# Kernel tuning notes

Measured on AMD Instinct MI355X. Metric: run time of the kernel, lower is better.

The kernel has to match this reference:

```python
import jax, jax.numpy as jnp
import numpy as np

B = 1024
P = 8
D = 2048
NUM_IDS = 64
MARGIN = 0.3
EPS = 1e-12


def setup_inputs() -> dict:
    key = jax.random.key(0)
    k1, k2, k3 = jax.random.split(key, 3)
    feats = jax.random.normal(k1, (B, P * D), dtype=jnp.float32)
    labels = jax.random.randint(k2, (B,), 0, NUM_IDS, dtype=jnp.int64)
    subs = jax.random.randint(k3, (B,), 0, 2, dtype=jnp.int64)
    return {"feats": feats, "labels": labels, "subs": subs}


def reference(feats, labels, subs):
    b = feats.shape[0]
    f = feats.reshape(b, -1, D)  # [B, P, D]
    dt = f.dtype

    # Per-sample class centers via a single segment-mean pass
    # (equivalent to the original per-sample boolean-mask mean loop).
    seg_sum = jax.ops.segment_sum(f, labels, num_segments=NUM_IDS)  # [NUM_IDS, P, D]
    counts = jax.ops.segment_sum(jnp.ones((b,), dt), labels, num_segments=NUM_IDS)
    centers_by_id = seg_sum / jnp.maximum(counts, 1.0)[:, None, None]
    centers = centers_by_id[labels]  # [B, P, D]

    # dist_ap[i] = sum_p ||f[i,p] - center[i,p]||
    d_ap = jnp.sqrt(jnp.clip(jnp.sum((f - centers) ** 2, axis=-1), EPS, None)).sum(-1)  # [B]
    dist_ap = d_ap[:, None] + d_ap[None, :]  # [B, B]

    # pairwise_distance: dist_aa[i,j] = sum_p ||f[i,p] - f[j,p]||, via gemm trick
    sq = jnp.sum(f * f, axis=-1)  # [B, P]
    inner = jnp.einsum('ipd,jpd->ijp', f, f)  # [B, B, P]
    d2 = sq[:, None, :] + sq[None, :, :] - 2.0 * inner
    dist_aa = jnp.sqrt(jnp.clip(d2, EPS, None)).sum(-1)  # [B, B]

    # masked margin loss over negative (different-label) pairs
    mask = labels[:, None] != labels[None, :]  # [B, B] bool
    vals = jnp.clip(dist_ap - dist_aa + MARGIN, 0.0, None)
    maskf = mask.astype(dt)
    loss = jnp.sum(vals * maskf) / jnp.sum(maskf)
    return loss
```

## Files before the change

### kernel.cpp

```cpp
#include <hip/hip_runtime.h>
#include <hip/hip_bf16.h>

#define B_ 1024
#define P_ 8
#define D_ 2048
#define FD_ (P_ * D_)
#define NID 64
#define MARGIN_ 0.3f
#define EPS_ 1e-12f

typedef unsigned short u16;
typedef float float4_t __attribute__((ext_vector_type(4)));

#define AS1 __attribute__((address_space(1)))
#define AS3 __attribute__((address_space(3)))

__device__ __forceinline__ float bf2f(u16 v) {
    unsigned x = (unsigned)v << 16;
    float f;
    __builtin_memcpy(&f, &x, 4);
    return f;
}

static const size_t OFF_COUNTS = 0;
static const size_t OFF_OFFS   = 256;
static const size_t OFF_PERM   = 512;
static const size_t OFF_NEG    = 4608;
static const size_t OFF_DONE   = 4616;
static const size_t OFF_POS    = 8176;
static const size_t OFF_S      = 8192;
static const size_t OFF_SQ     = 40960;
static const size_t OFF_DAP    = 73728;
static const size_t OFF_FB     = 131072;
static const size_t OFF_PD     = OFF_FB + (size_t)B_ * FD_;

__global__ void k_prep(const float* __restrict__ feats, const int* __restrict__ labels,
                       unsigned char* __restrict__ fb, float* __restrict__ sq,
                       float* countsf, int* offs, int* perm, float* negcnt,
                       float* S, float* possum, int* done) {
    int tid = threadIdx.x;
    if (blockIdx.x < B_) {
        int i = blockIdx.x;
        int w = tid >> 6, lane = tid & 63;
        const float* frow = feats + (size_t)i * FD_;
        unsigned char* brow = fb + (size_t)i * FD_;
#pragma unroll
        for (int pp = 0; pp < 2; pp++) {
            int p = w * 2 + pp;
            int off = p * D_;
            float s2 = 0.f;
#pragma unroll
            for (int ch = 0; ch < 8; ch++) {
                int d = off + ch * 256 + lane * 4;
                float4 f = *(const float4*)(frow + d);
                int pk = __builtin_amdgcn_cvt_pk_fp8_f32(f.x, f.y, 0, false);
                pk = __builtin_amdgcn_cvt_pk_fp8_f32(f.z, f.w, pk, true);
                *(unsigned int*)(brow + d) = (unsigned int)pk;
                s2 += f.x * f.x + f.y * f.y + f.z * f.z + f.w * f.w;
            }
            for (int o = 32; o; o >>= 1) s2 += __shfl_down(s2, o, 64);
            if (lane == 0) sq[i * P_ + p] = s2;
        }
        return;
    }
    __shared__ int h[NID], o[NID], cur[NID];
    if (tid < NID) h[tid] = 0;
    __syncthreads();
    for (int i = tid; i < B_; i += 256) atomicAdd(&h[labels[i]], 1);
    __syncthreads();
    if (tid == 0) {
        int acc = 0;
        long long ss = 0;
        for (int c = 0; c < NID; c++) {
            o[c] = acc;
            acc += h[c];
            ss += (long long)h[c] * h[c];
        }
        *negcnt = (float)((long long)B_ * B_ - ss);
        *possum = 0.f;
        done[0] = 0;
    }
    __syncthreads();
    if (tid < NID) {
        countsf[tid] = (float)h[tid];
        offs[tid] = o[tid];
        cur[tid] = o[tid];
    }
    __syncthreads();
    for (int i = tid; i < B_; i += 256) {
        int pos = atomicAdd(&cur[labels[i]], 1);
        perm[pos] = i;
    }
    for (int i = tid; i < B_ * P_; i += 256) S[i] = 0.f;
}

__global__ __launch_bounds__(256, 4) void k_pairs(const unsigned char* __restrict__ fb,
                                                  const float* __restrict__ sq,
                                                  const int* __restrict__ labels,
                                                  float* __restrict__ S,
                                                  u16* __restrict__ pd) {
    const int i0 = blockIdx.y * 128, j0 = blockIdx.x * 128;
    const int p = blockIdx.z;
    __shared__ __align__(16) unsigned char smem[32768];
    __shared__ float sqAs[128], sqBs[128];
    __shared__ int labA[128], labB[128];
    const int tid = threadIdx.x;
    const int lane = tid & 63, w = tid >> 6;
    const int wr = w >> 1, wc = w & 1;
    if (tid < 128) {
        sqAs[tid] = sq[(i0 + tid) * 8 + p];
        labA[tid] = labels[i0 + tid];
    } else {
        int t = tid - 128;
        sqBs[t] = sq[(j0 + t) * 8 + p];
        labB[t] = labels[j0 + t];
    }

    const int lhi = lane >> 4, llo = lane & 15;
    const int sl = llo & 7;
    const int lr = lane >> 3;
    const int lc = (lane & 7) ^ lr;

    unsigned char* const As = smem;
    unsigned char* const Bs = smem + 16384;

    const size_t colbase = (size_t)p * D_ + (size_t)lc * 16;
    const unsigned char* gA[4];
    const unsigned char* gB[4];
    unsigned char* lA[4];
    unsigned char* lB[4];
#pragma unroll
    for (int inst = 0; inst < 4; inst++) {
        int r0 = w * 32 + inst * 8;
        gA[inst] = fb + (size_t)(i0 + r0 + lr) * FD_ + colbase;
        gB[inst] = fb + (size_t)(j0 + r0 + lr) * FD_ + colbase;
        lA[inst] = As + r0 * 128;
        lB[inst] = Bs + r0 * 128;
    }

    float4_t acc[4][4];
#pragma unroll
    for (int a = 0; a < 4; a++)
#pragma unroll
        for (int b = 0; b < 4; b++) acc[a][b] = (float4_t){0.f, 0.f, 0.f, 0.f};

    for (int kb = 0; kb < 16; kb++) {
        const int koff = kb * 128;
        __syncthreads();
#pragma unroll
        for (int inst = 0; inst < 4; inst++) {
            __builtin_amdgcn_global_load_lds((const AS1 void*)(gA[inst] + koff),
                                             (AS3 void*)lA[inst], 16, 0, 0);
            __builtin_amdgcn_global_load_lds((const AS1 void*)(gB[inst] + koff),
                                             (AS3 void*)lB[inst], 16, 0, 0);
        }
        __syncthreads();
#pragma unroll
        for (int ks = 0; ks < 4; ks++) {
            const int pcb = ((2 * ks + (lhi >> 1)) ^ sl) * 16 + (lhi & 1) * 8;
            long af[4], bf[4];
#pragma unroll
            for (int a = 0; a < 4; a++) {
                af[a] = *(const long*)(As + (wr * 64 + a * 16 + llo) * 128 + pcb);
                bf[a] = *(const long*)(Bs + (wc * 64 + a * 16 + llo) * 128 + pcb);
            }
#pragma unroll
            for (int a = 0; a < 4; a++)
#pragma unroll
                for (int b = 0; b < 4; b++)
                    acc[a][b] = __builtin_amdgcn_mfma_f32_16x16x32_fp8_fp8(
                        af[a], bf[b], acc[a][b], 0, 0, 0);
        }
    }

    u16* outp = pd + (size_t)p * B_ * B_;
    float rs[4][4];
#pragma unroll
    for (int a = 0; a < 4; a++)
#pragma unroll
        for (int r = 0; r < 4; r++) rs[a][r] = 0.f;
#pragma unroll
    for (int a = 0; a < 4; a++) {
        int la0 = labA[wr * 64 + a * 16 + lhi * 4 + 0];
        int la1 = labA[wr * 64 + a * 16 + lhi * 4 + 1];
        int la2 = labA[wr * 64 + a * 16 + lhi * 4 + 2];
        int la3 = labA[wr * 64 + a * 16 + lhi * 4 + 3];
#pragma unroll
        for (int b = 0; b < 4; b++) {
            int jl = wc * 64 + b * 16 + llo;
            int lb = labB[jl];
#pragma unroll
            for (int r = 0; r < 4; r++) {
                int il = wr * 64 + a * 16 + lhi * 4 + r;
                float tt = acc[a][b][r];
                float d2 = sqAs[il] + sqBs[jl] - 2.0f * tt;
                outp[(size_t)(i0 + il) * B_ + (j0 + jl)] =
                    __bfloat16_as_ushort(__float2bfloat16(sqrtf(fmaxf(d2, EPS_))));
                int la = (r == 0) ? la0 : (r == 1) ? la1 : (r == 2) ? la2 : la3;
                if (lb == la) rs[a][r] += tt;
            }
        }
    }
#pragma unroll
    for (int a = 0; a < 4; a++)
#pragma unroll
        for (int r = 0; r < 4; r++) {
            float v = rs[a][r];
            v += __shfl_xor(v, 1, 64);
            v += __shfl_xor(v, 2, 64);
            v += __shfl_xor(v, 4, 64);
            v += __shfl_xor(v, 8, 64);
            if (llo == 0)
                atomicAdd(&S[(size_t)(i0 + wr * 64 + a * 16 + lhi * 4 + r) * 8 + p], v);
        }
}

__global__ void k_dap(const float* __restrict__ S, const float* __restrict__ sq,
                      const float* __restrict__ countsf, const int* __restrict__ offs,
                      const int* __restrict__ perm, float* __restrict__ dap) {
    int c = blockIdx.x;
    int tid = threadIdx.x;
    int cnt = (int)countsf[c];
    int off = offs[c];
    __shared__ float T[8];
    if (tid < 8) {
        float t = 0.f;
        for (int m = 0; m < cnt; m++) t += S[(size_t)perm[off + m] * 8 + tid];
        T[tid] = t;
    }
    __syncthreads();
    float n = fmaxf((float)cnt, 1.f);
    float inv = 1.f / n, inv2 = inv * inv;
    for (int m = tid; m < cnt; m += 64) {
        int i = perm[off + m];
        float d = 0.f;
#pragma unroll
        for (int p = 0; p < 8; p++) {
            float d2 = sq[i * 8 + p] - 2.f * inv * S[(size_t)i * 8 + p] + inv2 * T[p];
            d += sqrtf(fmaxf(d2, EPS_));
        }
        dap[i] = d;
    }
}

__global__ void k_lossred(const u16* __restrict__ pd, const float* __restrict__ dap,
                          const int* __restrict__ labels, float* possum,
                          const float* __restrict__ negcnt, int* __restrict__ done,
                          float* __restrict__ out) {
    int i = blockIdx.x;
    int tid = threadIdx.x;
    float di = dap[i];
    int li = labels[i];
    int j0 = tid * 4;
    float d0 = 0.f, d1 = 0.f, d2 = 0.f, d3 = 0.f;
#pragma unroll
    for (int p = 0; p < P_; p++) {
        ushort4 v = *(const ushort4*)&pd[(size_t)p * B_ * B_ + (size_t)i * B_ + j0];
        d0 += bf2f(v.x);
        d1 += bf2f(v.y);
        d2 += bf2f(v.z);
        d3 += bf2f(v.w);
    }
    int4 lj = *(const int4*)&labels[j0];
    float4 dj = *(const float4*)&dap[j0];
    float lsum = 0.f;
    if (lj.x != li) lsum += fmaxf(di + dj.x - d0 + MARGIN_, 0.f);
    if (lj.y != li) lsum += fmaxf(di + dj.y - d1 + MARGIN_, 0.f);
    if (lj.z != li) lsum += fmaxf(di + dj.z - d2 + MARGIN_, 0.f);
    if (lj.w != li) lsum += fmaxf(di + dj.w - d3 + MARGIN_, 0.f);
    for (int o = 32; o; o >>= 1) lsum += __shfl_down(lsum, o, 64);
    __shared__ float red[4];
    int wid = tid >> 6, lane = tid & 63;
    if (lane == 0) red[wid] = lsum;
    __syncthreads();
    if (tid == 0) {
        atomicAdd(possum, red[0] + red[1] + red[2] + red[3]);
        __threadfence();
        int v = atomicAdd(done, 1);
        if (v == B_ - 1) {
            float ps = atomicAdd(possum, 0.f);
            out[0] = ps / negcnt[0];
        }
    }
}

extern "C" void kernel_launch(void* const* d_in, const int* in_sizes, int n_in,
                              void* d_out, int out_size, void* d_ws, size_t ws_size,
                              hipStream_t stream) {
    const float* feats = (const float*)d_in[0];
    const int* labels  = (const int*)d_in[1];
    float* out = (float*)d_out;

    char* w = (char*)d_ws;
    float* countsf = (float*)(w + OFF_COUNTS);
    int* offs      = (int*)(w + OFF_OFFS);
    int* perm      = (int*)(w + OFF_PERM);
    float* negcnt  = (float*)(w + OFF_NEG);
    int* done      = (int*)(w + OFF_DONE);
    float* possum  = (float*)(w + OFF_POS);
    float* S       = (float*)(w + OFF_S);
    float* sq      = (float*)(w + OFF_SQ);
    float* dap     = (float*)(w + OFF_DAP);
    unsigned char* fb = (unsigned char*)(w + OFF_FB);
    u16* pd        = (u16*)(w + OFF_PD);

    k_prep<<<B_ + 1, 256, 0, stream>>>(feats, labels, fb, sq, countsf, offs, perm,
                                       negcnt, S, possum, done);
    k_pairs<<<dim3(8, 8, 8), 256, 0, stream>>>(fb, sq, labels, S, pd);
    k_dap<<<NID, 64, 0, stream>>>(S, sq, countsf, offs, perm, dap);
    k_lossred<<<B_, 256, 0, stream>>>(pd, dap, labels, possum, negcnt, done, out);
}
```

Measured before the change: 167.8 us.

## Double-buffer LDS tiles in pair GEMM and flatten grid with part-major ordering

The fp8 MFMA pairwise kernel now uses two 32KB LDS buffers, issuing the async global-to-LDS load for the next K-slice while computing on the current one, with one barrier per slice instead of two. The 3D grid is flattened so consecutive blocks walk the part index first, which changes scheduling order and likely L2 locality. Launch bounds drop to 2 blocks per CU to match the doubled shared memory, which lowers occupancy in exchange for overlap.

```diff
diff --git a/kernel.cpp b/kernel.cpp
--- a/kernel.cpp
+++ b/kernel.cpp
@@ -94,14 +94,17 @@
     for (int i = tid; i < B_ * P_; i += 256) S[i] = 0.f;
 }
 
-__global__ __launch_bounds__(256, 4) void k_pairs(const unsigned char* __restrict__ fb,
+__global__ __launch_bounds__(256, 2) void k_pairs(const unsigned char* __restrict__ fb,
                                                   const float* __restrict__ sq,
                                                   const int* __restrict__ labels,
                                                   float* __restrict__ S,
                                                   u16* __restrict__ pd) {
-    const int i0 = blockIdx.y * 128, j0 = blockIdx.x * 128;
-    const int p = blockIdx.z;
-    __shared__ __align__(16) unsigned char smem[32768];
+    const int bid = blockIdx.x;
+    const int p = bid & 7;
+    const int t = bid >> 3;
+    const int i0 = (t >> 3) * 128, j0 = (t & 7) * 128;
+
+    __shared__ __align__(16) unsigned char smem[65536];
     __shared__ float sqAs[128], sqBs[128];
     __shared__ int labA[128], labB[128];
     const int tid = threadIdx.x;
@@ -111,9 +114,9 @@
         sqAs[tid] = sq[(i0 + tid) * 8 + p];
         labA[tid] = labels[i0 + tid];
     } else {
-        int t = tid - 128;
-        sqBs[t] = sq[(j0 + t) * 8 + p];
-        labB[t] = labels[j0 + t];
+        int u = tid - 128;
+        sqBs[u] = sq[(j0 + u) * 8 + p];
+        labB[u] = labels[j0 + u];
     }
 
     const int lhi = lane >> 4, llo = lane & 15;
@@ -144,34 +147,55 @@
 #pragma unroll
         for (int b = 0; b < 4; b++) acc[a][b] = (float4_t){0.f, 0.f, 0.f, 0.f};
 
-    for (int kb = 0; kb < 16; kb++) {
-        const int koff = kb * 128;
+#define STAGE(BUF, KB)                                                                    \
+    {                                                                                     \
+        const int koff_ = (KB) * 128;                                                     \
+        _Pragma("unroll") for (int inst = 0; inst < 4; inst++) {                          \
+            __builtin_amdgcn_global_load_lds((const AS1 void*)(gA[inst] + koff_),         \
+                                             (AS3 void*)(lA[inst] + (BUF) * 32768),       \
+                                             16, 0, 0);                                   \
+            __builtin_amdgcn_global_load_lds((const AS1 void*)(gB[inst] + koff_),         \
+                                             (AS3 void*)(lB[inst] + (BUF) * 32768),       \
+                                             16, 0, 0);                                   \
+        }                                                                                 \
+    }
+
+#define COMPUTE(BUF)                                                                      \
+    {                                                                                     \
+        _Pragma("unroll") for (int ks = 0; ks < 4; ks++) {                                \
+            const int pcb = ((2 * ks + (lhi >> 1)) ^ sl) * 16 + (lhi & 1) * 8;            \
+            long af[4], bf[4];                                                            \
+            _Pragma("unroll") for (int a = 0; a < 4; a++) {                               \
+                af[a] = *(const long*)(As + (BUF) * 32768 +                               \
+                                       (wr * 64 + a * 16 + llo) * 128 + pcb);             \
+                bf[a] = *(const long*)(Bs + (BUF) * 32768 +                               \
+                                       (wc * 64 + a * 16 + llo) * 128 + pcb);             \
+            }                                                                             \
+            _Pragma("unroll") for (int a = 0; a < 4; a++)                                 \
+                _Pragma("unroll") for (int b = 0; b < 4; b++)                             \
+                    acc[a][b] = __builtin_amdgcn_mfma_f32_16x16x32_fp8_fp8(               \
+                        af[a], bf[b], acc[a][b], 0, 0, 0);                                \
+        }                                                                                 \
+    }
+
+    STAGE(0, 0);
+    __syncthreads();
+#pragma unroll 1
+    for (int kb2 = 0; kb2 < 7; kb2++) {
+        STAGE(1, 2 * kb2 + 1);
+        COMPUTE(0);
         __syncthreads();
-#pragma unroll
-        for (int inst = 0; inst < 4; inst++) {
-            __builtin_amdgcn_global_load_lds((const AS1 void*)(gA[inst] + koff),
-                                             (AS3 void*)lA[inst], 16, 0, 0);
-            __builtin_amdgcn_global_load_lds((const AS1 void*)(gB[inst] + koff),
-                                             (AS3 void*)lB[inst], 16, 0, 0);
-        }
+        STAGE(0, 2 * kb2 + 2);
+        COMPUTE(1);
         __syncthreads();
-#pragma unroll
-        for (int ks = 0; ks < 4; ks++) {
-            const int pcb = ((2 * ks + (lhi >> 1)) ^ sl) * 16 + (lhi & 1) * 8;
-            long af[4], bf[4];
-#pragma unroll
-            for (int a = 0; a < 4; a++) {
-                af[a] = *(const long*)(As + (wr * 64 + a * 16 + llo) * 128 + pcb);
-                bf[a] = *(const long*)(Bs + (wc * 64 + a * 16 + llo) * 128 + pcb);
-            }
-#pragma unroll
-            for (int a = 0; a < 4; a++)
-#pragma unroll
-                for (int b = 0; b < 4; b++)
-                    acc[a][b] = __builtin_amdgcn_mfma_f32_16x16x32_fp8_fp8(
-                        af[a], bf[b], acc[a][b], 0, 0, 0);
-        }
-    }
+    }
+    STAGE(1, 15);
+    COMPUTE(0);
+    __syncthreads();
+    COMPUTE(1);
+
+#undef STAGE
+#undef COMPUTE
 
     u16* outp = pd + (size_t)p * B_ * B_;
     float rs[4][4];
@@ -306,7 +330,7 @@
 
     k_prep<<<B_ + 1, 256, 0, stream>>>(feats, labels, fb, sq, countsf, offs, perm,
                                        negcnt, S, possum, done);
-    k_pairs<<<dim3(8, 8, 8), 256, 0, stream>>>(fb, sq, labels, S, pd);
+    k_pairs<<<512, 256, 0, stream>>>(fb, sq, labels, S, pd);
     k_dap<<<NID, 64, 0, stream>>>(S, sq, countsf, offs, perm, dap);
     k_lossred<<<B_, 256, 0, stream>>>(pd, dap, labels, possum, negcnt, done, out);
 }
```

Result: no change. 168.5 us (+0.4%).
